# Performance work log

Hardware: AMD Instinct MI355X
Metric: run time of the kernel (lower is better)

The kernel has to match this reference:

```python
import jax, jax.numpy as jnp
import numpy as np

B, H, S, D = 2048, 1024, 32768, 64  # batch, hidden_dim, memory_slots, slot_size


def setup_inputs() -> dict:
    key = jax.random.key(0)
    ks = jax.random.split(key, 8)
    inp = {
        "query": jax.random.normal(ks[0], (B, H), jnp.float32),
        "consciousness_level": jax.random.uniform(ks[1], (B,), jnp.float32),
        "content": jax.random.normal(ks[2], (B, H), jnp.float32),
        "memory": jax.random.normal(ks[3], (S, D), jnp.float32) * 0.1,
        "memory_age": jnp.zeros((S,), jnp.float32),
        "memory_strength": jnp.ones((S,), jnp.float32) * 0.1,
        "W_read": jax.random.normal(ks[4], (H + 1, S), jnp.float32) / np.sqrt(H + 1),
        "b_read": jnp.zeros((S,), jnp.float32),
        "W_write": jax.random.normal(ks[5], (H + 1, S), jnp.float32) / np.sqrt(H + 1),
        "b_write": jnp.zeros((S,), jnp.float32),
        "W_cp": jax.random.normal(ks[6], (H, D), jnp.float32) / np.sqrt(H),
        "b_cp": jnp.zeros((D,), jnp.float32),
        "W_ce": jax.random.normal(ks[7], (D, H), jnp.float32) / np.sqrt(D),
        "b_ce": jnp.zeros((H,), jnp.float32),
    }
    return inp


def reference(query, consciousness_level, content, memory, memory_age,
              memory_strength, W_read, b_read, W_write, b_write,
              W_cp, b_cp, W_ce, b_ce):
    # ---- read path ----
    enhanced_query = jnp.concatenate([query, consciousness_level[:, None]], axis=-1)  # [B, H+1]
    read_weights = jax.nn.softmax(enhanced_query @ W_read + b_read, axis=-1)          # [B, S]
    boosted = read_weights * memory_strength[None, :]
    boosted = boosted / (boosted.sum(axis=-1, keepdims=True) + 1e-6)
    read_content = boosted @ memory                                                   # [B, D]
    consciousness_boost = read_content @ W_ce + b_ce                                  # [B, H]

    # ---- write path (vectorized masked consolidation over all slots) ----
    c_mean = consciousness_level.mean()
    write_weights = jax.nn.softmax(enhanced_query @ W_write + b_write, axis=-1)       # [B, S]
    ww_mean = write_weights.mean(axis=0)                                              # [S]
    pc_mean = (content @ W_cp + b_cp).mean(axis=0)                                    # [D]
    weight = ww_mean * (c_mean * 2.0)                                                 # [S]
    gate = c_mean >= 0.3                                                              # auto-activation threshold
    mask = (weight > 0.005) & gate                                                    # [S] bool
    consolidation = jax.nn.sigmoid(memory_age * 0.1 + c_mean)                         # [S]
    alpha = weight * consolidation                                                    # [S]
    new_memory = jnp.where(mask[:, None],
                           (1.0 - alpha)[:, None] * memory + alpha[:, None] * pc_mean[None, :],
                           memory)                                                    # [S, D]
    new_age = memory_age + mask.astype(memory_age.dtype)
    new_strength = jnp.where(mask,
                             jnp.clip(memory_strength + weight * 0.1, 0.1, 2.0),
                             memory_strength)
    return read_content, consciousness_boost, new_memory, new_age, new_strength
```

## Files before the change

kernel.cpp:

```cpp
#include <hip/hip_runtime.h>
#include <hip/hip_bf16.h>
#include <cstdint>
#include <cstddef>

#define B_ 2048
#define H_ 1024
#define S_ 32768
#define D_ 64
#define BT 32
#define KP 1088
#define NT 17

typedef unsigned char u8;
typedef unsigned short u16;
typedef __attribute__((ext_vector_type(8))) short bf16x8;
typedef __attribute__((ext_vector_type(8))) unsigned short ushort8v;
typedef __attribute__((ext_vector_type(4))) float f32x4;

#define WS_CMEAN      0
#define WS_PCMEAN     64
#define WS_CMM        128
#define WS_ZR         (WS_CMM + H_)
#define WS_TR         (WS_ZR + B_)
#define WS_VR         (WS_TR + B_)
#define WS_ZW         (WS_VR + B_*D_)
#define WS_WWM        (WS_ZW + B_)
#define WS_END        (WS_WWM + S_)

__device__ __forceinline__ u16 f2bf(float f) {
  unsigned u = __float_as_uint(f);
  unsigned r = (u + 0x7FFFu + ((u >> 16) & 1u)) >> 16;
  return (u16)r;
}

__device__ __forceinline__ float bf2f(u16 v) {
  return __uint_as_float(((unsigned)v) << 16);
}

__device__ __forceinline__ u8 f8enc(float f) {
  f = fminf(f, 448.f);
  unsigned u = __float_as_uint(f);
  int ex = (int)((u >> 23) & 255) - 127;
  unsigned r;
  if (ex >= -6) {
    unsigned m = u & 0x7FFFFF;
    unsigned rm = (m + 0x7FFFF + ((m >> 20) & 1)) >> 20;
    r = ((unsigned)(ex + 7) << 3) + rm;
  } else {
    r = (unsigned)fminf(7.f, f * 512.f + 0.5f);
  }
  return (u8)(r > 126 ? 126 : r);
}

__device__ __forceinline__ float f8dec(u8 b) {
  int ef = (b >> 3) & 15, m = b & 7;
  return ef ? __uint_as_float(((unsigned)(ef + 120) << 23) | ((unsigned)m << 20))
            : (float)m * 0.001953125f;
}

__device__ __forceinline__ void gload_lds16(const void* g, void* l) {
  __builtin_amdgcn_global_load_lds(
      (const __attribute__((address_space(1))) unsigned int*)g,
      (__attribute__((address_space(3))) unsigned int*)l, 16, 0, 0);
}

__global__ void k_stats(const float* __restrict__ content,
                        const float* __restrict__ cl, float* __restrict__ ws) {
  const int gx = blockIdx.x, gy = blockIdx.y, t = threadIdx.x;
  if (gx < 4) {
    const int h = gx * 256 + t;
    const int b0 = gy * 64;
    float acc = 0.f;
    #pragma unroll 8
    for (int b = 0; b < 64; ++b) acc += content[(size_t)(b0 + b) * H_ + h];
    atomicAdd(&ws[WS_CMM + h], acc * (1.0f / B_));
  } else if (t < 64) {
    float acc = cl[gy * 64 + t];
    #pragma unroll
    for (int off = 32; off > 0; off >>= 1) acc += __shfl_down(acc, off);
    if (t == 0) atomicAdd(&ws[WS_CMEAN], acc * (1.0f / B_));
  }
}

__global__ void k_pcmean(const float* __restrict__ Wcp, const float* __restrict__ bcp,
                         float* __restrict__ ws) {
  __shared__ float red[16][64];
  const int t = threadIdx.x, d = t & 63, kk = t >> 6;
  float acc = 0.f;
  const int k0 = kk * 64;
  #pragma unroll 8
  for (int k = k0; k < k0 + 64; ++k)
    acc = fmaf(ws[WS_CMM + k], Wcp[(size_t)k * D_ + d], acc);
  red[kk][d] = acc;
  __syncthreads();
  if (t < 64) {
    float a = bcp[t];
    #pragma unroll
    for (int i = 0; i < 16; ++i) a += red[i][t];
    ws[WS_PCMEAN + t] = a;
  }
}


__global__ void k_cvt_qm(const float* __restrict__ query, const float* __restrict__ cl,
                         const float* __restrict__ mem,
                         u16* __restrict__ qb, u16* __restrict__ mT) {
  const int t = threadIdx.x;
  if (blockIdx.x < B_) {
    const int b = blockIdx.x;
    const float c = cl[b];
    #pragma unroll
    for (int i = 0; i < 5; ++i) {
      const int k = i * 256 + t;
      if (k < KP) {
        float v;
        if (k < H_) v = query[(size_t)b * H_ + k];
        else if (k == H_) v = c;
        else if (k == H_ + 1) v = 1.0f;
        else v = 0.f;
        qb[(size_t)b * KP + k] = f2bf(v);
      }
    }
  } else {
    __shared__ float tile[64][65];
    const int s0 = (blockIdx.x - B_) * 64;
    const int c = t & 63, rbase = t >> 6;
    #pragma unroll
    for (int i = 0; i < 16; ++i) {
      const int r = rbase + i * 4;
      tile[r][c] = mem[(size_t)(s0 + r) * D_ + c];
    }
    __syncthreads();
    #pragma unroll
    for (int i = 0; i < 16; ++i) {
      const int d = rbase + i * 4;
      mT[(size_t)d * S_ + s0 + c] = f2bf(tile[c][d]);
    }
  }
}

__global__ void k_cvt_wt(const float* __restrict__ W, const float* __restrict__ bias,
                         u16* __restrict__ wbt) {
  __shared__ float tile[64][65];
  const int t = threadIdx.x;
  const int s0 = blockIdx.x * 64;
  const int k0 = blockIdx.y * 64;
  const int c = t & 63, rbase = t >> 6;
  #pragma unroll
  for (int i = 0; i < 16; ++i) {
    const int r = rbase + i * 4;
    const int k = k0 + r;
    float v = 0.f;
    if (k <= H_) v = W[(size_t)k * S_ + s0 + c];
    else if (k == H_ + 1) v = bias[s0 + c];
    tile[r][c] = v;
  }
  __syncthreads();
  #pragma unroll
  for (int i = 0; i < 16; ++i) {
    const int sr = rbase + i * 4;
    const int k = k0 + c;
    if (k < KP) wbt[(size_t)(s0 + sr) * KP + k] = f2bf(tile[c][sr]);
  }
}

template <int NF>
__device__ __forceinline__ void rd_frags(const u16* __restrict__ lds, int rowbase,
                                         int lr, int lg, bf16x8 (&dst)[NF * 2]) {
  #pragma unroll
  for (int f = 0; f < NF; ++f) {
    const int rr = rowbase + f * 16 + lr;
    #pragma unroll
    for (int ks = 0; ks < 2; ++ks) {
      const int ch = (ks * 4 + lg) ^ (rr & 7);
      dst[f * 2 + ks] = *(const bf16x8*)&lds[rr * 64 + ch * 8];
    }
  }
}

template <int QR, int QC>
__device__ __forceinline__ void mfmaq(f32x4 (&acc)[8][4], const bf16x8 (&av)[8],
                                      const bf16x8 (&bv)[4]) {
  #pragma unroll
  for (int m16 = 0; m16 < 4; ++m16)
    #pragma unroll
    for (int n16 = 0; n16 < 2; ++n16)
      #pragma unroll
      for (int ks = 0; ks < 2; ++ks)
        acc[QR * 4 + m16][QC * 2 + n16] = __builtin_amdgcn_mfma_f32_16x16x32_bf16(
            av[m16 * 2 + ks], bv[n16 * 2 + ks], acc[QR * 4 + m16][QC * 2 + n16], 0, 0, 0);
}

template <int VARIANT>
__global__ __launch_bounds__(512, 2) void k_gemm(
    const u16* __restrict__ qb, const u16* __restrict__ wbt,
    const float* __restrict__ strength, const u16* __restrict__ mT,
    void* __restrict__ pout, float* __restrict__ ws) {
  __shared__ __align__(16) u16 SMEM[4][256 * 64];
  const int t = threadIdx.x;
  const int w = t >> 6, l = t & 63;
  const int wm = w >> 2, wn = w & 3;
  const int lr = l & 15, lg = l >> 4;

  const int lin = blockIdx.x + 8 * blockIdx.y;
  const int xcd = lin & 7, idx = lin >> 3;
  const size_t r0 = (size_t)(idx & 7) * 256;
  const int cblk = xcd * 16 + (idx >> 3);
  const size_t c0 = (size_t)cblk * 256;

  f32x4 acc[8][4];
  #pragma unroll
  for (int m = 0; m < 8; ++m)
    #pragma unroll
    for (int n = 0; n < 4; ++n) acc[m][n] = (f32x4)0.f;

  auto STAGE = [&](int kt2, int pp) {
    #pragma unroll
    for (int i = 0; i < 4; ++i) {
      const int q = i * 512 + t;
      const int r = q >> 3;
      const int sc = (q & 7) ^ (r & 7);
      gload_lds16(qb + (r0 + r) * KP + (size_t)kt2 * 64 + sc * 8, &SMEM[pp][q * 8]);
    }
    #pragma unroll
    for (int i = 0; i < 4; ++i) {
      const int q = i * 512 + t;
      const int r = q >> 3;
      const int sc = (q & 7) ^ (r & 7);
      gload_lds16(wbt + (c0 + r) * KP + (size_t)kt2 * 64 + sc * 8, &SMEM[2 + pp][q * 8]);
    }
  };

  STAGE(0, 0);
  STAGE(1, 1);
  asm volatile("s_waitcnt vmcnt(8)" ::: "memory");
  __builtin_amdgcn_sched_barrier(0);
  __builtin_amdgcn_s_barrier();

  for (int kt = 0; kt < NT; ++kt) {
    const int p = kt & 1;
    const u16* __restrict__ Ap = &SMEM[p][0];
    const u16* __restrict__ Bp = &SMEM[2 + p][0];
    bf16x8 a[8], b0[4], b1[4];
    rd_frags<4>(Ap, wm * 128 + 0, lr, lg, a);
    rd_frags<2>(Bp, wn * 64 + 0, lr, lg, b0);
    __builtin_amdgcn_sched_barrier(0);
    __builtin_amdgcn_s_barrier();
    __builtin_amdgcn_s_setprio(1);
    mfmaq<0, 0>(acc, a, b0);
    __builtin_amdgcn_s_setprio(0);
    __builtin_amdgcn_s_barrier();
    rd_frags<2>(Bp, wn * 64 + 32, lr, lg, b1);
    __builtin_amdgcn_sched_barrier(0);
    __builtin_amdgcn_s_barrier();
    __builtin_amdgcn_s_setprio(1);
    mfmaq<0, 1>(acc, a, b1);
    __builtin_amdgcn_s_setprio(0);
    __builtin_amdgcn_s_barrier();
    rd_frags<4>(Ap, wm * 128 + 64, lr, lg, a);
    __builtin_amdgcn_sched_barrier(0);
    __builtin_amdgcn_s_barrier();
    __builtin_amdgcn_s_setprio(1);
    mfmaq<1, 1>(acc, a, b1);
    __builtin_amdgcn_s_setprio(0);
    __builtin_amdgcn_s_barrier();
    if (kt + 2 < NT) STAGE(kt + 2, p);
    __builtin_amdgcn_s_barrier();
    __builtin_amdgcn_s_setprio(1);
    mfmaq<1, 0>(acc, a, b0);
    __builtin_amdgcn_s_setprio(0);
    if (kt + 2 < NT) {
      asm volatile("s_waitcnt vmcnt(8)" ::: "memory");
    } else if (kt + 1 < NT) {
      asm volatile("s_waitcnt vmcnt(0)" ::: "memory");
    }
    __builtin_amdgcn_sched_barrier(0);
    __builtin_amdgcn_s_barrier();
  }

  u16* __restrict__ Plds = &SMEM[0][0];

  if (VARIANT == 0) {
    float st4[4];
    #pragma unroll
    for (int n = 0; n < 4; ++n) st4[n] = strength[c0 + wn * 64 + n * 16 + lr];
    #pragma unroll
    for (int m = 0; m < 8; ++m) {
      #pragma unroll
      for (int j = 0; j < 4; ++j) {
        const int rloc = wm * 128 + m * 16 + lg * 4 + j;
        float ze = 0.f, zp = 0.f;
        #pragma unroll
        for (int n = 0; n < 4; ++n) {
          const float e = __expf(acc[m][n][j]);
          const float pq = e * st4[n];
          ze += e;
          zp += pq;
          const int col = wn * 64 + n * 16 + lr;
          const int ch = (col >> 3) ^ (rloc & 7);
          Plds[rloc * 256 + ch * 8 + (col & 7)] = f2bf(pq);
        }
        #pragma unroll
        for (int off = 1; off < 16; off <<= 1) {
          ze += __shfl_xor(ze, off);
          zp += __shfl_xor(zp, off);
        }
        if (lr == 0) {
          atomicAdd(&ws[WS_ZR + r0 + rloc], ze);
          atomicAdd(&ws[WS_TR + r0 + rloc], zp);
        }
      }
    }
    __syncthreads();
    float* __restrict__ vp = (float*)pout;
    f32x4 pv[2][4];
    #pragma unroll
    for (int f = 0; f < 2; ++f)
      #pragma unroll
      for (int n = 0; n < 4; ++n) pv[f][n] = (f32x4)0.f;
    #pragma unroll 2
    for (int ks = 0; ks < 8; ++ks) {
      bf16x8 pa[2], pb[4];
      #pragma unroll
      for (int f = 0; f < 2; ++f) {
        const int row = w * 32 + f * 16 + lr;
        const int ch = (ks * 4 + lg) ^ (row & 7);
        pa[f] = *(const bf16x8*)&Plds[row * 256 + ch * 8];
      }
      #pragma unroll
      for (int n = 0; n < 4; ++n)
        pb[n] = *(const bf16x8*)&mT[(size_t)(n * 16 + lr) * S_ + c0 + ks * 32 + lg * 8];
      #pragma unroll
      for (int f = 0; f < 2; ++f)
        #pragma unroll
        for (int n = 0; n < 4; ++n)
          pv[f][n] = __builtin_amdgcn_mfma_f32_16x16x32_bf16(pa[f], pb[n], pv[f][n], 0, 0, 0);
    }
    #pragma unroll
    for (int f = 0; f < 2; ++f) {
      #pragma unroll
      for (int j = 0; j < 4; ++j) {
        const size_t R = (size_t)cblk * B_ + r0 + w * 32 + f * 16 + lg * 4 + j;
        #pragma unroll
        for (int n = 0; n < 4; ++n)
          vp[R * 64 + n * 16 + lr] = pv[f][n][j];
      }
    }
  } else {
    #pragma unroll
    for (int m = 0; m < 8; ++m) {
      #pragma unroll
      for (int j = 0; j < 4; ++j) {
        const int rloc = wm * 128 + m * 16 + lg * 4 + j;
        #pragma unroll
        for (int n = 0; n < 4; ++n) {
          const int col = wn * 64 + n * 16 + lr;
          const int ch = (col >> 3) ^ (rloc & 7);
          Plds[rloc * 256 + ch * 8 + (col & 7)] = f2bf(__expf(acc[m][n][j]));
        }
      }
    }
    __syncthreads();
    u8* __restrict__ pout8 = (u8*)pout;
    #pragma unroll 2
    for (int it = 0; it < 8; ++it) {
      const int row = w * 32 + it * 4 + (l >> 4);
      const int c2 = (l & 15) * 2;
      const bf16x8 e0 = *(const bf16x8*)&Plds[row * 256 + ((c2 ^ (row & 7)) * 8)];
      const bf16x8 e1 = *(const bf16x8*)&Plds[row * 256 + (((c2 + 1) ^ (row & 7)) * 8)];
      float ze = 0.f;
      uint4 fb;
      unsigned wds[4] = {0, 0, 0, 0};
      #pragma unroll
      for (int q = 0; q < 8; ++q) {
        const float ea = bf2f((u16)e0[q]);
        const float eb = bf2f((u16)e1[q]);
        ze += ea + eb;
        wds[q >> 2] |= ((unsigned)f8enc(ea)) << ((q & 3) * 8);
        wds[2 + (q >> 2)] |= ((unsigned)f8enc(eb)) << ((q & 3) * 8);
      }
      fb.x = wds[0]; fb.y = wds[1]; fb.z = wds[2]; fb.w = wds[3];
      *(uint4*)&pout8[(r0 + row) * S_ + c0 + (size_t)(l & 15) * 16] = fb;
      #pragma unroll
      for (int off = 1; off < 16; off <<= 1) ze += __shfl_xor(ze, off);
      if ((l & 15) == 0) atomicAdd(&ws[WS_ZW + r0 + row], ze);
    }
  }
}

__global__ void k_rc2(const float* __restrict__ vp, const float* __restrict__ ws,
                      float* __restrict__ out) {
  const int idx = blockIdx.x * 256 + threadIdx.x;
  const int b = idx >> 6;
  float v = 0.f;
  #pragma unroll 4
  for (int c = 0; c < 128; ++c) v += vp[(size_t)c * B_ * 64 + idx];
  const float inv = 1.0f / (ws[WS_TR + b] + 1e-6f * ws[WS_ZR + b]);
  out[idx] = v * inv;
}


__global__ void k_wwm_f8(const u8* __restrict__ ebuf, float* __restrict__ ws) {
  const int t = threadIdx.x;
  const int s0 = blockIdx.x * 4096 + t * 16;
  const int b0 = blockIdx.y * 128;
  float ww[16];
  #pragma unroll
  for (int j = 0; j < 16; ++j) ww[j] = 0.f;
  #pragma unroll 1
  for (int b = 0; b < 128; ++b) {
    const float inv = 1.0f / ws[WS_ZW + b0 + b];
    const uint4 v = *reinterpret_cast<const uint4*>(&ebuf[(size_t)(b0 + b) * S_ + s0]);
    const unsigned vv[4] = {v.x, v.y, v.z, v.w};
    #pragma unroll
    for (int j = 0; j < 16; ++j) {
      const u8 byte = (u8)((vv[j >> 2] >> ((j & 3) * 8)) & 0xFF);
      ww[j] = fmaf(f8dec(byte), inv, ww[j]);
    }
  }
  #pragma unroll
  for (int j = 0; j < 16; ++j) atomicAdd(&ws[WS_WWM + s0 + j], ww[j]);
}

__global__ void k_rc(const float* __restrict__ ws, float* __restrict__ out) {
  const int idx = blockIdx.x * 256 + threadIdx.x;
  const int b = idx >> 6;
  const float z = ws[WS_ZR + b], tt = ws[WS_TR + b];
  out[idx] = ws[WS_VR + idx] / (tt + 1e-6f * z);
}

__global__ void k_cboost(const float* __restrict__ rc, const float* __restrict__ Wce,
                         const float* __restrict__ bce, float* __restrict__ out) {
  const int idx = blockIdx.x * 256 + threadIdx.x;
  const int b = idx >> 10, h = idx & 1023;
  const float* __restrict__ rcb = &rc[b * 64];
  float acc = bce[h];
  #pragma unroll
  for (int dd = 0; dd < 64; dd += 4) {
    const float4 r4 = *reinterpret_cast<const float4*>(&rcb[dd]);
    acc = fmaf(r4.x, Wce[(size_t)(dd + 0) * H_ + h], acc);
    acc = fmaf(r4.y, Wce[(size_t)(dd + 1) * H_ + h], acc);
    acc = fmaf(r4.z, Wce[(size_t)(dd + 2) * H_ + h], acc);
    acc = fmaf(r4.w, Wce[(size_t)(dd + 3) * H_ + h], acc);
  }
  out[idx] = acc;
}

__global__ void k_final(const float* __restrict__ mem, const float* __restrict__ age,
                        const float* __restrict__ strength, const float* __restrict__ ws,
                        float* __restrict__ out_mem, float* __restrict__ out_age,
                        float* __restrict__ out_str) {
  const int idx = blockIdx.x * 256 + threadIdx.x;
  const int s = idx >> 6, dd = idx & 63;
  const float cm = ws[WS_CMEAN];
  const float w = ws[WS_WWM + s] * (2.0f * cm / B_);
  const bool mask = (w > 0.005f) && (cm >= 0.3f);
  float m = mem[idx];
  if (mask) {
    const float cons = 1.0f / (1.0f + __expf(-(age[s] * 0.1f + cm)));
    const float alpha = w * cons;
    m = (1.0f - alpha) * m + alpha * ws[WS_PCMEAN + dd];
  }
  out_mem[idx] = m;
  if (dd == 0) {
    out_age[s] = age[s] + (mask ? 1.0f : 0.0f);
    out_str[s] = mask ? fminf(fmaxf(strength[s] + w * 0.1f, 0.1f), 2.0f) : strength[s];
  }
}


template <int NR>
__device__ __forceinline__ void logits_kloop(const float* __restrict__ q, int row0,
                                             const float* __restrict__ W, int s,
                                             float* acc) {
  #pragma unroll 1
  for (int k = 0; k < H_; k += 4) {
    const float w0 = W[(size_t)(k + 0) * S_ + s];
    const float w1 = W[(size_t)(k + 1) * S_ + s];
    const float w2 = W[(size_t)(k + 2) * S_ + s];
    const float w3 = W[(size_t)(k + 3) * S_ + s];
    #pragma unroll
    for (int r = 0; r < NR; ++r) {
      const float4 qv = *reinterpret_cast<const float4*>(&q[(size_t)(row0 + r) * H_ + k]);
      float a = acc[r];
      a = fmaf(qv.x, w0, a);
      a = fmaf(qv.y, w1, a);
      a = fmaf(qv.z, w2, a);
      a = fmaf(qv.w, w3, a);
      acc[r] = a;
    }
  }
}

__global__ __launch_bounds__(512, 2) void k_read(
    const float* __restrict__ q, const float* __restrict__ cl,
    const float* __restrict__ Wr, const float* __restrict__ br,
    const float* __restrict__ strength, const float* __restrict__ mem,
    float* __restrict__ ws) {
  __shared__ float plds[BT * 512];
  const int t = threadIdx.x;
  const int r0 = blockIdx.x * BT;
  const int squar = blockIdx.y;
  const int d = t & 63, wv = t >> 6;

  float zacc[BT], tacc[BT];
  #pragma unroll
  for (int r = 0; r < BT; ++r) { zacc[r] = 0.f; tacc[r] = 0.f; }
  float vacc[4] = {0.f, 0.f, 0.f, 0.f};

  for (int tile = 0; tile < 16; ++tile) {
    const int sg0 = squar * 8192 + tile * 512;
    const int s = sg0 + t;
    float acc[BT];
    const float wlast = Wr[(size_t)H_ * S_ + s];
    const float bias = br[s];
    #pragma unroll
    for (int r = 0; r < BT; ++r) acc[r] = fmaf(cl[r0 + r], wlast, bias);
    logits_kloop<BT>(q, r0, Wr, s, acc);

    const float stg = strength[s];
    #pragma unroll
    for (int r = 0; r < BT; ++r) {
      const float e = __expf(acc[r]);
      zacc[r] += e;
      const float p = e * stg;
      tacc[r] += p;
      plds[r * 512 + t] = p;
    }
    __syncthreads();
    #pragma unroll 1
    for (int sl = 0; sl < 512; sl += 4) {
      const float m0 = mem[(size_t)(sg0 + sl + 0) * D_ + d];
      const float m1 = mem[(size_t)(sg0 + sl + 1) * D_ + d];
      const float m2 = mem[(size_t)(sg0 + sl + 2) * D_ + d];
      const float m3 = mem[(size_t)(sg0 + sl + 3) * D_ + d];
      #pragma unroll
      for (int j = 0; j < 4; ++j) {
        const float4 pv = *reinterpret_cast<const float4*>(&plds[(wv + 8 * j) * 512 + sl]);
        float v = vacc[j];
        v = fmaf(pv.x, m0, v);
        v = fmaf(pv.y, m1, v);
        v = fmaf(pv.z, m2, v);
        v = fmaf(pv.w, m3, v);
        vacc[j] = v;
      }
    }
    __syncthreads();
  }

  float* red0 = plds;
  float* red1 = plds + 8 * BT;
  #pragma unroll
  for (int r = 0; r < BT; ++r) {
    float z = zacc[r], tt = tacc[r];
    #pragma unroll
    for (int off = 32; off > 0; off >>= 1) {
      z += __shfl_down(z, off);
      tt += __shfl_down(tt, off);
    }
    if ((t & 63) == 0) { red0[wv * BT + r] = z; red1[wv * BT + r] = tt; }
  }
  __syncthreads();
  if (t < BT) {
    float z = 0.f, tt = 0.f;
    #pragma unroll
    for (int wq = 0; wq < 8; ++wq) { z += red0[wq * BT + t]; tt += red1[wq * BT + t]; }
    atomicAdd(&ws[WS_ZR + r0 + t], z);
    atomicAdd(&ws[WS_TR + r0 + t], tt);
  }
  #pragma unroll
  for (int j = 0; j < 4; ++j)
    atomicAdd(&ws[WS_VR + (size_t)(r0 + wv + 8 * j) * D_ + d], vacc[j]);
}

__global__ __launch_bounds__(512, 2) void k_write_pass1(
    const float* __restrict__ q, const float* __restrict__ cl,
    const float* __restrict__ Ww, const float* __restrict__ bw,
    float* __restrict__ ws, __hip_bfloat16* __restrict__ ebuf, const int store_e) {
  __shared__ float red[8 * BT];
  const int t = threadIdx.x;
  const int r0 = blockIdx.x * BT;
  const int squar = blockIdx.y;
  const int wv = t >> 6;

  float zacc[BT];
  #pragma unroll
  for (int r = 0; r < BT; ++r) zacc[r] = 0.f;

  for (int tile = 0; tile < 16; ++tile) {
    const int s = squar * 8192 + tile * 512 + t;
    float acc[BT];
    const float wlast = Ww[(size_t)H_ * S_ + s];
    const float bias = bw[s];
    #pragma unroll
    for (int r = 0; r < BT; ++r) acc[r] = fmaf(cl[r0 + r], wlast, bias);
    logits_kloop<BT>(q, r0, Ww, s, acc);
    #pragma unroll
    for (int r = 0; r < BT; ++r) {
      const float e = __expf(acc[r]);
      zacc[r] += e;
      if (store_e) ebuf[(size_t)(r0 + r) * S_ + s] = __float2bfloat16(e);
    }
  }
  #pragma unroll
  for (int r = 0; r < BT; ++r) {
    float z = zacc[r];
    #pragma unroll
    for (int off = 32; off > 0; off >>= 1) z += __shfl_down(z, off);
    if ((t & 63) == 0) red[wv * BT + r] = z;
  }
  __syncthreads();
  if (t < BT) {
    float z = 0.f;
    #pragma unroll
    for (int wq = 0; wq < 8; ++wq) z += red[wq * BT + t];
    atomicAdd(&ws[WS_ZW + r0 + t], z);
  }
}

__global__ void k_wwm_store(const __hip_bfloat16* __restrict__ ebuf,
                            float* __restrict__ ws) {
  const int t = threadIdx.x;
  const int s0 = blockIdx.x * 2048 + t * 8;
  const int b0 = blockIdx.y * 128;
  const u16* __restrict__ eb = (const u16*)ebuf;
  float ww[8];
  #pragma unroll
  for (int j = 0; j < 8; ++j) ww[j] = 0.f;
  #pragma unroll 1
  for (int b = 0; b < 128; ++b) {
    const float inv = 1.0f / ws[WS_ZW + b0 + b];
    const ushort8v ev = *reinterpret_cast<const ushort8v*>(&eb[(size_t)(b0 + b) * S_ + s0]);
    #pragma unroll
    for (int j = 0; j < 8; ++j) {
      const float e = __uint_as_float(((unsigned)ev[j]) << 16);
      ww[j] = fmaf(e, inv, ww[j]);
    }
  }
  #pragma unroll
  for (int j = 0; j < 8; ++j) atomicAdd(&ws[WS_WWM + s0 + j], ww[j]);
}

__global__ __launch_bounds__(512, 2) void k_wwm_recompute(
    const float* __restrict__ q, const float* __restrict__ cl,
    const float* __restrict__ Ww, const float* __restrict__ bw,
    float* __restrict__ ws) {
  const int t = threadIdx.x;
  const int s = blockIdx.x * 512 + t;
  const int b0 = blockIdx.y * 256;
  const float wlast = Ww[(size_t)H_ * S_ + s];
  const float bias = bw[s];
  float wwacc = 0.f;
  for (int g = 0; g < 8; ++g) {
    const int rb = b0 + g * 32;
    float acc[BT];
    #pragma unroll
    for (int r = 0; r < BT; ++r) acc[r] = fmaf(cl[rb + r], wlast, bias);
    logits_kloop<BT>(q, rb, Ww, s, acc);
    #pragma unroll
    for (int r = 0; r < BT; ++r) wwacc += __expf(acc[r]) / ws[WS_ZW + rb + r];
  }
  atomicAdd(&ws[WS_WWM + s], wwacc);
}


extern "C" void kernel_launch(void* const* d_in, const int* in_sizes, int n_in,
                              void* d_out, int out_size, void* d_ws, size_t ws_size,
                              hipStream_t stream) {
  const float* query    = (const float*)d_in[0];
  const float* cl       = (const float*)d_in[1];
  const float* content  = (const float*)d_in[2];
  const float* memory   = (const float*)d_in[3];
  const float* age      = (const float*)d_in[4];
  const float* strength = (const float*)d_in[5];
  const float* W_read   = (const float*)d_in[6];
  const float* b_read   = (const float*)d_in[7];
  const float* W_write  = (const float*)d_in[8];
  const float* b_write  = (const float*)d_in[9];
  const float* W_cp     = (const float*)d_in[10];
  const float* b_cp     = (const float*)d_in[11];
  const float* W_ce     = (const float*)d_in[12];
  const float* b_ce     = (const float*)d_in[13];

  float* out = (float*)d_out;
  float* ws = (float*)d_ws;
  float* out_rc  = out;
  float* out_cb  = out + B_ * D_;
  float* out_mem = out_cb + (size_t)B_ * H_;
  float* out_age = out_mem + (size_t)S_ * D_;
  float* out_str = out_age + S_;

  const size_t QB_F   = WS_END;
  const size_t MEMT_F = QB_F + (size_t)B_ * KP / 2;
  const size_t WBT_F  = MEMT_F + (size_t)D_ * S_ / 2;
  const size_t PBUF_F = WBT_F + (size_t)S_ * KP / 2;
  const size_t FAST_END_F = PBUF_F + (size_t)128 * B_ * 64;

  hipMemsetAsync(ws, 0, (size_t)WS_END * sizeof(float), stream);
  k_stats<<<dim3(5, 32), 256, 0, stream>>>(content, cl, ws);
  k_pcmean<<<1, 1024, 0, stream>>>(W_cp, b_cp, ws);

  if (ws_size >= FAST_END_F * sizeof(float)) {
    u16* qb   = (u16*)(ws + QB_F);
    u16* mT   = (u16*)(ws + MEMT_F);
    u16* wbt  = (u16*)(ws + WBT_F);
    float* vp = (float*)(ws + PBUF_F);
    u8*  pf8  = (u8*)(ws + PBUF_F);

    k_cvt_qm<<<B_ + S_ / 64, 256, 0, stream>>>(query, cl, memory, qb, mT);
    k_cvt_wt<<<dim3(S_ / 64, KP / 64), 256, 0, stream>>>(W_read, b_read, wbt);
    k_gemm<0><<<dim3(8, 128), 512, 0, stream>>>(qb, wbt, strength, mT, (void*)vp, ws);
    k_rc2<<<(B_ * D_) / 256, 256, 0, stream>>>(vp, ws, out_rc);
    k_cboost<<<(B_ * H_) / 256, 256, 0, stream>>>(out_rc, W_ce, b_ce, out_cb);
    k_cvt_wt<<<dim3(S_ / 64, KP / 64), 256, 0, stream>>>(W_write, b_write, wbt);
    k_gemm<1><<<dim3(8, 128), 512, 0, stream>>>(qb, wbt, nullptr, mT, (void*)pf8, ws);
    k_wwm_f8<<<dim3(8, 16), 256, 0, stream>>>(pf8, ws);
    k_final<<<(S_ * D_) / 256, 256, 0, stream>>>(memory, age, strength, ws,
                                                 out_mem, out_age, out_str);
  } else {
    const size_t ebuf_bytes = (size_t)B_ * S_ * 2;
    const int store_e = (ws_size >= (size_t)WS_END * 4 + ebuf_bytes) ? 1 : 0;
    __hip_bfloat16* ebuf = (__hip_bfloat16*)(ws + WS_END);

    k_read<<<dim3(B_ / BT, 4), 512, 0, stream>>>(query, cl, W_read, b_read, strength, memory, ws);
    k_write_pass1<<<dim3(B_ / BT, 4), 512, 0, stream>>>(query, cl, W_write, b_write, ws, ebuf, store_e);
    k_rc<<<(B_ * D_) / 256, 256, 0, stream>>>(ws, out_rc);
    k_cboost<<<(B_ * H_) / 256, 256, 0, stream>>>(out_rc, W_ce, b_ce, out_cb);
    if (store_e) {
      k_wwm_store<<<dim3(S_ / 2048, B_ / 128), 256, 0, stream>>>(ebuf, ws);
    } else {
      k_wwm_recompute<<<dim3(S_ / 512, 8), 512, 0, stream>>>(query, cl, W_write, b_write, ws);
    }
    k_final<<<(S_ * D_) / 256, 256, 0, stream>>>(memory, age, strength, ws,
                                                 out_mem, out_age, out_str);
  }
}
```

Before: 735.7 us.

## Fuse preprocessing kernels and fold bias/consciousness column into GEMM epilogue

Merges stats, query/memory conversion and both weight transposes into one k_pre launch. The GEMM K dimension shrinks from 1088 to 1024, and the rank-1 consciousness term and bias are added in fp32 in the epilogue instead of as padded bf16 columns. k_rc2 is fused with k_cboost and the pc_mean reduction, which cuts launches and the K-padding work. The cost is a second bf16 weight buffer in the workspace and an extra epilogue load per tile.

```diff
diff --git a/kernel.cpp b/kernel.cpp
--- a/kernel.cpp
+++ b/kernel.cpp
@@ -8,8 +8,9 @@
 #define S_ 32768
 #define D_ 64
 #define BT 32
+#define KQ 1024
+#define NT 16
 #define KP 1088
-#define NT 17
 
 typedef unsigned char u8;
 typedef unsigned short u16;
@@ -64,66 +65,37 @@
       (__attribute__((address_space(3))) unsigned int*)l, 16, 0, 0);
 }
 
-__global__ void k_stats(const float* __restrict__ content,
-                        const float* __restrict__ cl, float* __restrict__ ws) {
-  const int gx = blockIdx.x, gy = blockIdx.y, t = threadIdx.x;
-  if (gx < 4) {
-    const int h = gx * 256 + t;
-    const int b0 = gy * 64;
+
+__global__ void k_pre(const float* __restrict__ query, const float* __restrict__ cl,
+                      const float* __restrict__ content, const float* __restrict__ mem,
+                      const float* __restrict__ Wr, const float* __restrict__ Ww,
+                      u16* __restrict__ qb, u16* __restrict__ mT,
+                      u16* __restrict__ wbtR, u16* __restrict__ wbtW,
+                      float* __restrict__ ws) {
+  const int blk = blockIdx.x, t = threadIdx.x;
+  if (blk < 128) {
+    const int h = (blk & 3) * 256 + t;
+    const int b0 = (blk >> 2) * 64;
     float acc = 0.f;
     #pragma unroll 8
     for (int b = 0; b < 64; ++b) acc += content[(size_t)(b0 + b) * H_ + h];
     atomicAdd(&ws[WS_CMM + h], acc * (1.0f / B_));
-  } else if (t < 64) {
-    float acc = cl[gy * 64 + t];
-    #pragma unroll
-    for (int off = 32; off > 0; off >>= 1) acc += __shfl_down(acc, off);
-    if (t == 0) atomicAdd(&ws[WS_CMEAN], acc * (1.0f / B_));
-  }
-}
-
-__global__ void k_pcmean(const float* __restrict__ Wcp, const float* __restrict__ bcp,
-                         float* __restrict__ ws) {
-  __shared__ float red[16][64];
-  const int t = threadIdx.x, d = t & 63, kk = t >> 6;
-  float acc = 0.f;
-  const int k0 = kk * 64;
-  #pragma unroll 8
-  for (int k = k0; k < k0 + 64; ++k)
-    acc = fmaf(ws[WS_CMM + k], Wcp[(size_t)k * D_ + d], acc);
-  red[kk][d] = acc;
-  __syncthreads();
-  if (t < 64) {
-    float a = bcp[t];
-    #pragma unroll
-    for (int i = 0; i < 16; ++i) a += red[i][t];
-    ws[WS_PCMEAN + t] = a;
-  }
-}
-
-
-__global__ void k_cvt_qm(const float* __restrict__ query, const float* __restrict__ cl,
-                         const float* __restrict__ mem,
-                         u16* __restrict__ qb, u16* __restrict__ mT) {
-  const int t = threadIdx.x;
-  if (blockIdx.x < B_) {
-    const int b = blockIdx.x;
-    const float c = cl[b];
-    #pragma unroll
-    for (int i = 0; i < 5; ++i) {
-      const int k = i * 256 + t;
-      if (k < KP) {
-        float v;
-        if (k < H_) v = query[(size_t)b * H_ + k];
-        else if (k == H_) v = c;
-        else if (k == H_ + 1) v = 1.0f;
-        else v = 0.f;
-        qb[(size_t)b * KP + k] = f2bf(v);
-      }
-    }
-  } else {
+  } else if (blk < 160) {
+    if (t < 64) {
+      float acc = cl[(blk - 128) * 64 + t];
+      #pragma unroll
+      for (int off = 32; off > 0; off >>= 1) acc += __shfl_down(acc, off);
+      if (t == 0) atomicAdd(&ws[WS_CMEAN], acc * (1.0f / B_));
+    }
+  } else if (blk < 160 + B_) {
+    const int b = blk - 160;
+    const float4 q4 = *reinterpret_cast<const float4*>(&query[(size_t)b * H_ + t * 4]);
+    ushort4 o;
+    o.x = f2bf(q4.x); o.y = f2bf(q4.y); o.z = f2bf(q4.z); o.w = f2bf(q4.w);
+    *reinterpret_cast<ushort4*>(&qb[(size_t)b * KQ + t * 4]) = o;
+  } else if (blk < 160 + B_ + 512) {
     __shared__ float tile[64][65];
-    const int s0 = (blockIdx.x - B_) * 64;
+    const int s0 = (blk - 160 - B_) * 64;
     const int c = t & 63, rbase = t >> 6;
     #pragma unroll
     for (int i = 0; i < 16; ++i) {
@@ -136,31 +108,27 @@
       const int d = rbase + i * 4;
       mT[(size_t)d * S_ + s0 + c] = f2bf(tile[c][d]);
     }
-  }
-}
-
-__global__ void k_cvt_wt(const float* __restrict__ W, const float* __restrict__ bias,
-                         u16* __restrict__ wbt) {
-  __shared__ float tile[64][65];
-  const int t = threadIdx.x;
-  const int s0 = blockIdx.x * 64;
-  const int k0 = blockIdx.y * 64;
-  const int c = t & 63, rbase = t >> 6;
-  #pragma unroll
-  for (int i = 0; i < 16; ++i) {
-    const int r = rbase + i * 4;
-    const int k = k0 + r;
-    float v = 0.f;
-    if (k <= H_) v = W[(size_t)k * S_ + s0 + c];
-    else if (k == H_ + 1) v = bias[s0 + c];
-    tile[r][c] = v;
-  }
-  __syncthreads();
-  #pragma unroll
-  for (int i = 0; i < 16; ++i) {
-    const int sr = rbase + i * 4;
-    const int k = k0 + c;
-    if (k < KP) wbt[(size_t)(s0 + sr) * KP + k] = f2bf(tile[c][sr]);
+  } else {
+    const int base = 160 + B_ + 512;
+    const int isW = blk >= base + 8192;
+    const int i = blk - base - (isW ? 8192 : 0);
+    const float* __restrict__ W = isW ? Ww : Wr;
+    u16* __restrict__ wbt = isW ? wbtW : wbtR;
+    __shared__ float tile[64][65];
+    const int s0 = (i & 511) * 64;
+    const int k0 = (i >> 9) * 64;
+    const int c = t & 63, rbase = t >> 6;
+    #pragma unroll
+    for (int j = 0; j < 16; ++j) {
+      const int r = rbase + j * 4;
+      tile[r][c] = W[(size_t)(k0 + r) * S_ + s0 + c];
+    }
+    __syncthreads();
+    #pragma unroll
+    for (int j = 0; j < 16; ++j) {
+      const int sr = rbase + j * 4;
+      wbt[(size_t)(s0 + sr) * KQ + k0 + c] = f2bf(tile[c][sr]);
+    }
   }
 }
 
@@ -194,8 +162,9 @@
 template <int VARIANT>
 __global__ __launch_bounds__(512, 2) void k_gemm(
     const u16* __restrict__ qb, const u16* __restrict__ wbt,
-    const float* __restrict__ strength, const u16* __restrict__ mT,
-    void* __restrict__ pout, float* __restrict__ ws) {
+    const float* __restrict__ Wfull, const float* __restrict__ biasv,
+    const float* __restrict__ cl, const float* __restrict__ strength,
+    const u16* __restrict__ mT, void* __restrict__ pout, float* __restrict__ ws) {
   __shared__ __align__(16) u16 SMEM[4][256 * 64];
   const int t = threadIdx.x;
   const int w = t >> 6, l = t & 63;
@@ -220,14 +189,14 @@
       const int q = i * 512 + t;
       const int r = q >> 3;
       const int sc = (q & 7) ^ (r & 7);
-      gload_lds16(qb + (r0 + r) * KP + (size_t)kt2 * 64 + sc * 8, &SMEM[pp][q * 8]);
+      gload_lds16(qb + (r0 + r) * KQ + (size_t)kt2 * 64 + sc * 8, &SMEM[pp][q * 8]);
     }
     #pragma unroll
     for (int i = 0; i < 4; ++i) {
       const int q = i * 512 + t;
       const int r = q >> 3;
       const int sc = (q & 7) ^ (r & 7);
-      gload_lds16(wbt + (c0 + r) * KP + (size_t)kt2 * 64 + sc * 8, &SMEM[2 + pp][q * 8]);
+      gload_lds16(wbt + (c0 + r) * KQ + (size_t)kt2 * 64 + sc * 8, &SMEM[2 + pp][q * 8]);
     }
   };
 
@@ -278,6 +247,24 @@
     __builtin_amdgcn_s_barrier();
   }
 
+  float wl4[4], bb4[4];
+  #pragma unroll
+  for (int n = 0; n < 4; ++n) {
+    const size_t col = c0 + wn * 64 + n * 16 + lr;
+    wl4[n] = Wfull[(size_t)H_ * S_ + col];
+    bb4[n] = biasv[col];
+  }
+  #pragma unroll
+  for (int m = 0; m < 8; ++m) {
+    #pragma unroll
+    for (int j = 0; j < 4; ++j) {
+      const float clv = cl[r0 + wm * 128 + m * 16 + lg * 4 + j];
+      #pragma unroll
+      for (int n = 0; n < 4; ++n)
+        acc[m][n][j] += fmaf(clv, wl4[n], bb4[n]);
+    }
+  }
+
   u16* __restrict__ Plds = &SMEM[0][0];
 
   if (VARIANT == 0) {
@@ -388,15 +375,56 @@
   }
 }
 
-__global__ void k_rc2(const float* __restrict__ vp, const float* __restrict__ ws,
-                      float* __restrict__ out) {
-  const int idx = blockIdx.x * 256 + threadIdx.x;
-  const int b = idx >> 6;
+__global__ void k_rc2cb(const float* __restrict__ vp, const float* __restrict__ Wcp,
+                        const float* __restrict__ bcp, const float* __restrict__ Wce,
+                        const float* __restrict__ bce, float* __restrict__ ws,
+                        float* __restrict__ out_rc, float* __restrict__ out_cb) {
+  const int t = threadIdx.x;
+  if (blockIdx.x == 512) {
+    __shared__ float red[4][64];
+    const int d = t & 63, kk = t >> 6;
+    float acc = 0.f;
+    #pragma unroll 8
+    for (int k = kk * 256; k < kk * 256 + 256; ++k)
+      acc = fmaf(ws[WS_CMM + k], Wcp[(size_t)k * D_ + d], acc);
+    red[kk][d] = acc;
+    __syncthreads();
+    if (t < 64) {
+      float a = bcp[t];
+      #pragma unroll
+      for (int i = 0; i < 4; ++i) a += red[i][t];
+      ws[WS_PCMEAN + t] = a;
+    }
+    return;
+  }
+  __shared__ float rcs[4][64];
+  const int idx = blockIdx.x * 256 + t;
+  const int b = idx >> 6, d = idx & 63;
   float v = 0.f;
   #pragma unroll 4
   for (int c = 0; c < 128; ++c) v += vp[(size_t)c * B_ * 64 + idx];
-  const float inv = 1.0f / (ws[WS_TR + b] + 1e-6f * ws[WS_ZR + b]);
-  out[idx] = v * inv;
+  const float rcv = v / (ws[WS_TR + b] + 1e-6f * ws[WS_ZR + b]);
+  out_rc[idx] = rcv;
+  rcs[t >> 6][d] = rcv;
+  __syncthreads();
+  const int b0 = blockIdx.x * 4;
+  #pragma unroll
+  for (int oo = 0; oo < 4; ++oo) {
+    const int h = oo * 256 + t;
+    float a0 = bce[h], a1 = a0, a2 = a0, a3 = a0;
+    #pragma unroll 8
+    for (int dd = 0; dd < 64; ++dd) {
+      const float wv = Wce[(size_t)dd * H_ + h];
+      a0 = fmaf(rcs[0][dd], wv, a0);
+      a1 = fmaf(rcs[1][dd], wv, a1);
+      a2 = fmaf(rcs[2][dd], wv, a2);
+      a3 = fmaf(rcs[3][dd], wv, a3);
+    }
+    out_cb[(size_t)(b0 + 0) * H_ + h] = a0;
+    out_cb[(size_t)(b0 + 1) * H_ + h] = a1;
+    out_cb[(size_t)(b0 + 2) * H_ + h] = a2;
+    out_cb[(size_t)(b0 + 3) * H_ + h] = a3;
+  }
 }
 
 
@@ -420,30 +448,6 @@
   }
   #pragma unroll
   for (int j = 0; j < 16; ++j) atomicAdd(&ws[WS_WWM + s0 + j], ww[j]);
-}
-
-__global__ void k_rc(const float* __restrict__ ws, float* __restrict__ out) {
-  const int idx = blockIdx.x * 256 + threadIdx.x;
-  const int b = idx >> 6;
-  const float z = ws[WS_ZR + b], tt = ws[WS_TR + b];
-  out[idx] = ws[WS_VR + idx] / (tt + 1e-6f * z);
-}
-
-__global__ void k_cboost(const float* __restrict__ rc, const float* __restrict__ Wce,
-                         const float* __restrict__ bce, float* __restrict__ out) {
-  const int idx = blockIdx.x * 256 + threadIdx.x;
-  const int b = idx >> 10, h = idx & 1023;
-  const float* __restrict__ rcb = &rc[b * 64];
-  float acc = bce[h];
-  #pragma unroll
-  for (int dd = 0; dd < 64; dd += 4) {
-    const float4 r4 = *reinterpret_cast<const float4*>(&rcb[dd]);
-    acc = fmaf(r4.x, Wce[(size_t)(dd + 0) * H_ + h], acc);
-    acc = fmaf(r4.y, Wce[(size_t)(dd + 1) * H_ + h], acc);
-    acc = fmaf(r4.z, Wce[(size_t)(dd + 2) * H_ + h], acc);
-    acc = fmaf(r4.w, Wce[(size_t)(dd + 3) * H_ + h], acc);
-  }
-  out[idx] = acc;
 }
 
 __global__ void k_final(const float* __restrict__ mem, const float* __restrict__ age,
@@ -469,6 +473,43 @@
 }
 
 
+__global__ void k_stats(const float* __restrict__ content,
+                        const float* __restrict__ cl, float* __restrict__ ws) {
+  const int gx = blockIdx.x, gy = blockIdx.y, t = threadIdx.x;
+  if (gx < 4) {
+    const int h = gx * 256 + t;
+    const int b0 = gy * 64;
+    float acc = 0.f;
+    #pragma unroll 8
+    for (int b = 0; b < 64; ++b) acc += content[(size_t)(b0 + b) * H_ + h];
+    atomicAdd(&ws[WS_CMM + h], acc * (1.0f / B_));
+  } else if (t < 64) {
+    float acc = cl[gy * 64 + t];
+    #pragma unroll
+    for (int off = 32; off > 0; off >>= 1) acc += __shfl_down(acc, off);
+    if (t == 0) atomicAdd(&ws[WS_CMEAN], acc * (1.0f / B_));
+  }
+}
+
+__global__ void k_pcmean(const float* __restrict__ Wcp, const float* __restrict__ bcp,
+                         float* __restrict__ ws) {
+  __shared__ float red[16][64];
+  const int t = threadIdx.x, d = t & 63, kk = t >> 6;
+  float acc = 0.f;
+  const int k0 = kk * 64;
+  #pragma unroll 8
+  for (int k = k0; k < k0 + 64; ++k)
+    acc = fmaf(ws[WS_CMM + k], Wcp[(size_t)k * D_ + d], acc);
+  red[kk][d] = acc;
+  __syncthreads();
+  if (t < 64) {
+    float a = bcp[t];
+    #pragma unroll
+    for (int i = 0; i < 16; ++i) a += red[i][t];
+    ws[WS_PCMEAN + t] = a;
+  }
+}
+
 template <int NR>
 __device__ __forceinline__ void logits_kloop(const float* __restrict__ q, int row0,
                                              const float* __restrict__ W, int s,
@@ -616,6 +657,30 @@
     for (int wq = 0; wq < 8; ++wq) z += red[wq * BT + t];
     atomicAdd(&ws[WS_ZW + r0 + t], z);
   }
+}
+
+__global__ void k_rc(const float* __restrict__ ws, float* __restrict__ out) {
+  const int idx = blockIdx.x * 256 + threadIdx.x;
+  const int b = idx >> 6;
+  const float z = ws[WS_ZR + b], tt = ws[WS_TR + b];
+  out[idx] = ws[WS_VR + idx] / (tt + 1e-6f * z);
+}
+
+__global__ void k_cboost(const float* __restrict__ rc, const float* __restrict__ Wce,
+                         const float* __restrict__ bce, float* __restrict__ out) {
+  const int idx = blockIdx.x * 256 + threadIdx.x;
+  const int b = idx >> 10, h = idx & 1023;
+  const float* __restrict__ rcb = &rc[b * 64];
+  float acc = bce[h];
+  #pragma unroll
+  for (int dd = 0; dd < 64; dd += 4) {
+    const float4 r4 = *reinterpret_cast<const float4*>(&rcb[dd]);
+    acc = fmaf(r4.x, Wce[(size_t)(dd + 0) * H_ + h], acc);
+    acc = fmaf(r4.y, Wce[(size_t)(dd + 1) * H_ + h], acc);
+    acc = fmaf(r4.z, Wce[(size_t)(dd + 2) * H_ + h], acc);
+    acc = fmaf(r4.w, Wce[(size_t)(dd + 3) * H_ + h], acc);
+  }
+  out[idx] = acc;
 }
 
 __global__ void k_wwm_store(const __hip_bfloat16* __restrict__ ebuf,
@@ -690,30 +755,30 @@
   float* out_age = out_mem + (size_t)S_ * D_;
   float* out_str = out_age + S_;
 
-  const size_t QB_F   = WS_END;
-  const size_t MEMT_F = QB_F + (size_t)B_ * KP / 2;
-  const size_t WBT_F  = MEMT_F + (size_t)D_ * S_ / 2;
-  const size_t PBUF_F = WBT_F + (size_t)S_ * KP / 2;
+  const size_t QB_F    = WS_END;
+  const size_t MEMT_F  = QB_F + (size_t)B_ * KQ / 2;
+  const size_t WBTR_F  = MEMT_F + (size_t)D_ * S_ / 2;
+  const size_t WBTW_F  = WBTR_F + (size_t)S_ * KQ / 2;
+  const size_t PBUF_F  = WBTW_F + (size_t)S_ * KQ / 2;
   const size_t FAST_END_F = PBUF_F + (size_t)128 * B_ * 64;
 
   hipMemsetAsync(ws, 0, (size_t)WS_END * sizeof(float), stream);
-  k_stats<<<dim3(5, 32), 256, 0, stream>>>(content, cl, ws);
-  k_pcmean<<<1, 1024, 0, stream>>>(W_cp, b_cp, ws);
 
   if (ws_size >= FAST_END_F * sizeof(float)) {
     u16* qb   = (u16*)(ws + QB_F);
     u16* mT   = (u16*)(ws + MEMT_F);
-    u16* wbt  = (u16*)(ws + WBT_F);
+    u16* wbtR = (u16*)(ws + WBTR_F);
+    u16* wbtW = (u16*)(ws + WBTW_F);
     float* vp = (float*)(ws + PBUF_F);
     u8*  pf8  = (u8*)(ws + PBUF_F);
 
-    k_cvt_qm<<<B_ + S_ / 64, 256, 0, stream>>>(query, cl, memory, qb, mT);
-    k_cvt_wt<<<dim3(S_ / 64, KP / 64), 256, 0, stream>>>(W_read, b_read, wbt);
-    k_gemm<0><<<dim3(8, 128), 512, 0, stream>>>(qb, wbt, strength, mT, (void*)vp, ws);
-    k_rc2<<<(B_ * D_) / 256, 256, 0, stream>>>(vp, ws, out_rc);
-    k_cboost<<<(B_ * H_) / 256, 256, 0, stream>>>(out_rc, W_ce, b_ce, out_cb);
-    k_cvt_wt<<<dim3(S_ / 64, KP / 64), 256, 0, stream>>>(W_write, b_write, wbt);
-    k_gemm<1><<<dim3(8, 128), 512, 0, stream>>>(qb, wbt, nullptr, mT, (void*)pf8, ws);
+    k_pre<<<160 + B_ + 512 + 2 * 8192, 256, 0, stream>>>(
+        query, cl, content, memory, W_read, W_write, qb, mT, wbtR, wbtW, ws);
+    k_gemm<0><<<dim3(8, 128), 512, 0, stream>>>(qb, wbtR, W_read, b_read, cl,
+                                                strength, mT, (void*)vp, ws);
+    k_rc2cb<<<513, 256, 0, stream>>>(vp, W_cp, b_cp, W_ce, b_ce, ws, out_rc, out_cb);
+    k_gemm<1><<<dim3(8, 128), 512, 0, stream>>>(qb, wbtW, W_write, b_write, cl,
+                                                nullptr, mT, (void*)pf8, ws);
     k_wwm_f8<<<dim3(8, 16), 256, 0, stream>>>(pf8, ws);
     k_final<<<(S_ * D_) / 256, 256, 0, stream>>>(memory, age, strength, ws,
                                                  out_mem, out_age, out_str);
@@ -722,6 +787,8 @@
     const int store_e = (ws_size >= (size_t)WS_END * 4 + ebuf_bytes) ? 1 : 0;
     __hip_bfloat16* ebuf = (__hip_bfloat16*)(ws + WS_END);
 
+    k_stats<<<dim3(5, 32), 256, 0, stream>>>(content, cl, ws);
+    k_pcmean<<<1, 1024, 0, stream>>>(W_cp, b_cp, ws);
     k_read<<<dim3(B_ / BT, 4), 512, 0, stream>>>(query, cl, W_read, b_read, strength, memory, ws);
     k_write_pass1<<<dim3(B_ / BT, 4), 512, 0, stream>>>(query, cl, W_write, b_write, ws, ebuf, store_e);
     k_rc<<<(B_ * D_) / 256, 256, 0, stream>>>(ws, out_rc);
```

Result: faster. 667.7 us (-9.2%).
